# Optimization experiments

Hardware: AMD Instinct MI355X
Metric: run time of the kernel (lower is better)

The kernel has to match this reference:

```python
import jax, jax.numpy as jnp
import numpy as np

B, S, HID = 2, 2048, 4096
H, P, N, G, K = 128, 64, 128, 8, 4      # heads, head_dim, ssm_state, groups, conv kernel
INTER = H * P                           # 8192
CONV_DIM = INTER + 2 * G * N            # 10240
CHUNK = 128
EPS = 1e-5
DT_MIN, DT_MAX = 0.0, 100.0


def setup_inputs() -> dict:
    key = jax.random.key(0)
    ks = jax.random.split(key, 4)
    proj = INTER + CONV_DIM + H
    return {
        "x": jax.random.normal(ks[0], (B, S, HID), jnp.float32),
        "in_proj_w": jax.random.normal(ks[1], (proj, HID), jnp.float32) * 0.02,
        "conv_w": jax.random.normal(ks[2], (CONV_DIM, 1, K), jnp.float32) * 0.2,
        "conv_b": jnp.zeros((CONV_DIM,), jnp.float32),
        "dt_bias": jnp.ones((H,), jnp.float32),
        "A_log": jnp.log(jnp.arange(1, H + 1, dtype=jnp.float32)),
        "D": jnp.ones((H,), jnp.float32),
        "norm_w": jnp.ones((INTER,), jnp.float32),
        "out_proj_w": jax.random.normal(ks[3], (HID, INTER), jnp.float32) * 0.02,
    }


def _segsum(a):
    # a: (..., c) -> (..., c, c); [i, j] = sum_{k=j+1..i} a[k] for i >= j, else -inf
    c = a.shape[-1]
    s = jnp.cumsum(a, axis=-1)
    diff = s[..., :, None] - s[..., None, :]
    mask = jnp.tril(jnp.ones((c, c), dtype=bool))
    return jnp.where(mask, diff, -jnp.inf)


def reference(x, in_proj_w, conv_w, conv_b, dt_bias, A_log, D, norm_w, out_proj_w):
    b, s, _ = x.shape
    proj = jnp.einsum('bsd,ed->bse', x, in_proj_w)
    gate = proj[..., :INTER]
    hBC = proj[..., INTER:INTER + CONV_DIM]
    dt = proj[..., INTER + CONV_DIM:]                       # (b, s, H)

    # depthwise causal conv1d + silu
    xc = jnp.transpose(hBC, (0, 2, 1))                      # (b, conv_dim, s)
    xc = jax.lax.conv_general_dilated(xc, conv_w, (1,), [(K - 1, 0)],
                                      dimension_numbers=('NCH', 'OIH', 'NCH'),
                                      feature_group_count=CONV_DIM)
    xc = xc + conv_b[None, :, None]
    hBC = jax.nn.silu(jnp.transpose(xc, (0, 2, 1)))

    hs = hBC[..., :INTER].reshape(b, s, H, P)
    Bm = hBC[..., INTER:INTER + G * N].reshape(b, s, G, N)
    Cm = hBC[..., INTER + G * N:].reshape(b, s, G, N)

    A = -jnp.exp(A_log)                                     # (H,)
    dt = jnp.clip(jax.nn.softplus(dt + dt_bias), DT_MIN, DT_MAX)

    rep = H // G
    Bh = jnp.repeat(Bm, rep, axis=2)                        # (b, s, H, N)
    Ch = jnp.repeat(Cm, rep, axis=2)

    nc = s // CHUNK
    xch = (hs * dt[..., None]).reshape(b, nc, CHUNK, H, P)  # dt-scaled input, chunked
    Bc = Bh.reshape(b, nc, CHUNK, H, N)
    Cc = Ch.reshape(b, nc, CHUNK, H, N)
    A_dt = (dt * A).reshape(b, nc, CHUNK, H).transpose(0, 3, 1, 2)  # (b, H, nc, c)
    A_cum = jnp.cumsum(A_dt, axis=-1)

    # intra-chunk (diagonal) contribution
    L = jnp.exp(_segsum(A_dt))                              # (b, H, nc, c, c)
    Y_diag = jnp.einsum('bzlhn,bzshn,bhzls,bzshp->bzlhp', Cc, Bc, L, xch)

    # per-chunk final states
    decay_states = jnp.exp(A_cum[..., -1:] - A_cum)         # (b, H, nc, c)
    states = jnp.einsum('bzlhn,bhzl,bzlhp->bzhpn', Bc, decay_states, xch)

    # inter-chunk recurrence (initial state = 0)
    states_p = jnp.concatenate([jnp.zeros_like(states[:, :1]), states], axis=1)  # (b, nc+1, H, P, N)
    A_last = jnp.pad(A_cum[..., -1], ((0, 0), (0, 0), (1, 0)))                   # (b, H, nc+1)
    decay_chunk = jnp.exp(_segsum(A_last))                                        # (b, H, nc+1, nc+1)
    new_states = jnp.einsum('bhzc,bchpn->bzhpn', decay_chunk, states_p)
    prev = new_states[:, :-1]                                # state entering each chunk

    Y_off = jnp.einsum('bzlhn,bzhpn,bhzl->bzlhp', Cc, prev, jnp.exp(A_cum))
    Y = (Y_diag + Y_off).reshape(b, s, H, P) + hs * D[None, None, :, None]
    y = Y.reshape(b, s, INTER)

    # gated grouped RMSNorm (norm_before_gate=False)
    g = y * jax.nn.silu(gate)
    gg = g.reshape(b, s, G, INTER // G)
    var = jnp.mean(gg * gg, axis=-1, keepdims=True)
    gg = gg * jax.lax.rsqrt(var + EPS)
    out = gg.reshape(b, s, INTER) * norm_w

    return jnp.einsum('bsi,oi->bso', out, out_proj_w)
```

## Files before the change

kernel.cpp:

```cpp
#include <hip/hip_runtime.h>
#include <hip/hip_bf16.h>
#include <cstdint>
#include <cstddef>

#define DEVI __device__ __forceinline__

#define BB 2
#define S_LEN 2048
#define HID_DIM 4096
#define NH 128
#define PD 64
#define NS 128
#define NG 8
#define INTER 8192
#define CONVD 10240
#define PROJ 18560
#define PROJP 18688
#define NC 16
#define BS 4096
#define GN 1024

using short8 = __attribute__((ext_vector_type(8))) short;
using short4v = __attribute__((ext_vector_type(4))) short;
using f32x4  = __attribute__((ext_vector_type(4))) float;
using bf16x8 = __attribute__((ext_vector_type(8))) __bf16;

DEVI float bf2f(short u) {
  union { unsigned int i; float f; } v;
  v.i = ((unsigned int)(unsigned short)u) << 16;
  return v.f;
}
DEVI short f2bf(float f) {
  union { float ff; unsigned int i; } v; v.ff = f;
  unsigned int x = v.i;
  return (short)((x + 0x7fffu + ((x >> 16) & 1u)) >> 16);
}
DEVI f32x4 mfma16(short8 a, short8 b, f32x4 c) {
  return __builtin_amdgcn_mfma_f32_16x16x32_bf16(
      __builtin_bit_cast(bf16x8, a), __builtin_bit_cast(bf16x8, b), c, 0, 0, 0);
}
DEVI void gl_lds16(const short* g, short* l) {
  __builtin_amdgcn_global_load_lds(
      (const __attribute__((address_space(1))) void*)g,
      (__attribute__((address_space(3))) void*)l, 16, 0, 0);
}
DEVI float sigmoidf_(float x) { return 1.f / (1.f + __expf(-x)); }

__global__ __launch_bounds__(256) void cvt_f32_bf16_k(const float* __restrict__ in,
                                                      short* __restrict__ out, size_t n) {
  size_t i = ((size_t)blockIdx.x * 256 + threadIdx.x) * 8;
  if (i + 8 > n) return;
  float4 a = *(const float4*)(in + i);
  float4 b = *(const float4*)(in + i + 4);
  short8 o;
  o[0] = f2bf(a.x); o[1] = f2bf(a.y); o[2] = f2bf(a.z); o[3] = f2bf(a.w);
  o[4] = f2bf(b.x); o[5] = f2bf(b.y); o[6] = f2bf(b.z); o[7] = f2bf(b.w);
  *(short8*)(out + i) = o;
}


#define STG(ISB, BUF, KH, TILE) do { \
  const short* _src = (ISB) ? Bt : A; \
  const int _r0 = (ISB) ? n0 : m0; \
  short* _lb = lds_ + ((ISB) ? 32768 : 0) + ((BUF)*2+(KH))*8192; \
  const int _kt = (TILE)*64 + (KH)*32; \
  { int _row = (wid*2)*16 + srow; int _sl = sps ^ ((_row>>1)&3); \
    gl_lds16(_src + (size_t)(_r0+_row)*K + _kt + _sl*8, _lb + (wid*2)*512); } \
  { int _row = (wid*2+1)*16 + srow; int _sl = sps ^ ((_row>>1)&3); \
    gl_lds16(_src + (size_t)(_r0+_row)*K + _kt + _sl*8, _lb + (wid*2+1)*512); } \
} while(0)

#define VM4 asm volatile("s_waitcnt vmcnt(4)" ::: "memory")
#define VM0 asm volatile("s_waitcnt vmcnt(0)" ::: "memory")

#define LDAF(DST, BUF, KH, MIH) do { \
  _Pragma("unroll") \
  for (int _m = 0; _m < 4; ++_m) { \
    int _row = wr*128 + ((MIH)*4+_m)*16 + fr; \
    DST[_m] = *(const short8*)(lds_ + ((BUF)*2+(KH))*8192 + _row*32 + ((slot ^ ((_row>>1)&3))<<3)); \
  } \
} while(0)

#define LDBF(DST, BUF, KH) do { \
  _Pragma("unroll") \
  for (int _n = 0; _n < 4; ++_n) { \
    int _row = wc*64 + _n*16 + fr; \
    DST[_n] = *(const short8*)(lds_ + 32768 + ((BUF)*2+(KH))*8192 + _row*32 + ((slot ^ ((_row>>1)&3))<<3)); \
  } \
} while(0)

#define MFMA16X(MIH, AF, BF) do { \
  _Pragma("unroll") \
  for (int _m = 0; _m < 4; ++_m) \
    _Pragma("unroll") \
    for (int _n = 0; _n < 4; ++_n) \
      acc[(MIH)*4+_m][_n] = mfma16(AF[_m], BF[_n], acc[(MIH)*4+_m][_n]); \
} while(0)

#define ITER(CB, NB, TNEXT, DOSTG, VMW) do { \
  if (DOSTG) { STG(0, NB, 0, TNEXT); STG(1, NB, 0, TNEXT); } \
  VMW; \
  __builtin_amdgcn_s_barrier(); \
  LDAF(af0, CB, 0, 0); LDAF(af1, CB, 1, 0); \
  LDBF(bf0, CB, 0); LDBF(bf1, CB, 1); \
  __builtin_amdgcn_s_setprio(1); \
  MFMA16X(0, af0, bf0); \
  MFMA16X(0, af1, bf1); \
  __builtin_amdgcn_s_setprio(0); \
  if (DOSTG) { STG(0, NB, 1, TNEXT); STG(1, NB, 1, TNEXT); } \
  LDAF(af0, CB, 0, 1); LDAF(af1, CB, 1, 1); \
  __builtin_amdgcn_s_setprio(1); \
  MFMA16X(1, af0, bf0); \
  MFMA16X(1, af1, bf1); \
  __builtin_amdgcn_s_setprio(0); \
  asm volatile("s_waitcnt lgkmcnt(0)" ::: "memory"); \
  __builtin_amdgcn_s_barrier(); \
} while(0)

template<int CB16>
__global__ __launch_bounds__(512, 2) void gemm256_k(const short* __restrict__ A,
                                                    const short* __restrict__ Bt,
                                                    void* __restrict__ Cout,
                                                    int Nstride, int K, int ntn) {
  __shared__ short lds_[65536];
  const int tid = threadIdx.x, wid = tid >> 6, lane = tid & 63;
  const int nwg = gridDim.x, orig = blockIdx.x;
  const int swz = (orig & 7) * (nwg >> 3) + (orig >> 3);
  const int per_group = ntn << 3;
  const int group = swz / per_group;
  const int rem = swz - group * per_group;
  const int m0 = (group * 8 + (rem & 7)) * 256;
  const int n0 = (rem >> 3) * 256;
  const int wr = wid >> 2, wc = wid & 3;
  const int fr = lane & 15, slot = lane >> 4;
  const int srow = lane >> 2, sps = lane & 3;

  f32x4 acc[8][4] = {};
  short8 af0[4], af1[4], bf0[4], bf1[4];
  const int NT = K >> 6;

  STG(0, 0, 0, 0); STG(1, 0, 0, 0); STG(0, 0, 1, 0); STG(1, 0, 1, 0);

  for (int ii = 0; ii < (NT >> 1) - 1; ++ii) {
    const int t = 2 * ii;
    ITER(0, 1, t + 1, 1, VM4);
    ITER(1, 0, t + 2, 1, VM4);
  }
  ITER(0, 1, NT - 1, 1, VM4);
  ITER(1, 0, 0, 0, VM0);

  const int er = (lane >> 4) * 4, ec = lane & 15;
  if (CB16) {
    short* C = (short*)Cout;
#pragma unroll
    for (int mi = 0; mi < 8; ++mi)
#pragma unroll
      for (int j = 0; j < 4; ++j) {
        size_t base = (size_t)(m0 + wr * 128 + mi * 16 + er + j) * Nstride + n0 + wc * 64 + ec;
#pragma unroll
        for (int ni = 0; ni < 4; ++ni) C[base + ni * 16] = f2bf(acc[mi][ni][j]);
      }
  } else {
    float* C = (float*)Cout;
#pragma unroll
    for (int mi = 0; mi < 8; ++mi)
#pragma unroll
      for (int j = 0; j < 4; ++j) {
        size_t base = (size_t)(m0 + wr * 128 + mi * 16 + er + j) * Nstride + n0 + wc * 64 + ec;
#pragma unroll
        for (int ni = 0; ni < 4; ++ni) C[base + ni * 16] = acc[mi][ni][j];
      }
  }
}

__global__ __launch_bounds__(256) void conv_silu_k(const short* __restrict__ projb,
                                                   const float* __restrict__ convw,
                                                   const float* __restrict__ convb,
                                                   short* __restrict__ hbc) {
  const int c = blockIdx.x * 256 + threadIdx.x;
  const int s0 = blockIdx.y * 256;
  const int b = blockIdx.z;
  const size_t rb = (size_t)b * S_LEN;
  const float* wp = convw + (size_t)c * 4;
  const float w0 = wp[0], w1 = wp[1], w2 = wp[2], w3 = wp[3];
  const float bias = convb[c];
  const short* pcol = projb + INTER + c;
  float x1 = 0.f, x2 = 0.f, x3 = 0.f;
  if (s0 > 0) {
    x3 = bf2f(pcol[(rb + s0 - 3) * PROJP]);
    x2 = bf2f(pcol[(rb + s0 - 2) * PROJP]);
    x1 = bf2f(pcol[(rb + s0 - 1) * PROJP]);
  }
  for (int s = s0; s < s0 + 256; ++s) {
    float v = bf2f(pcol[(rb + s) * PROJP]);
    float acc = bias + w0 * x3 + w1 * x2 + w2 * x1 + w3 * v;
    float o = acc * sigmoidf_(acc);
    hbc[(rb + s) * CONVD + c] = f2bf(o);
    x3 = x2; x2 = x1; x1 = v;
  }
}

__global__ __launch_bounds__(128) void acum_k(const short* __restrict__ projb,
                                              const float* __restrict__ dt_bias,
                                              const float* __restrict__ A_log,
                                              float* __restrict__ dtT,
                                              float* __restrict__ acum) {
  const int l = threadIdx.x;
  const int z = blockIdx.x, h = blockIdx.y, b = blockIdx.z;
  const float A = -__expf(A_log[h]);
  __shared__ float sv[128];
  const int r = b * S_LEN + z * 128 + l;
  float xv = bf2f(projb[(size_t)r * PROJP + INTER + CONVD + h]) + dt_bias[h];
  float sp = (xv > 20.f) ? xv : log1pf(__expf(xv));
  sp = fminf(fmaxf(sp, 0.f), 100.f);
  const size_t base = ((size_t)(b * NH + h)) * S_LEN + z * 128;
  dtT[base + l] = sp;
  sv[l] = sp * A;
  __syncthreads();
  for (int off = 1; off < 128; off <<= 1) {
    float t = (l >= off) ? sv[l - off] : 0.f;
    __syncthreads();
    sv[l] += t;
    __syncthreads();
  }
  acum[base + l] = sv[l];
}

__global__ __launch_bounds__(512) void states_k(const short* __restrict__ hbc,
                                                const float* __restrict__ dtT,
                                                const float* __restrict__ acum,
                                                float* __restrict__ states) {
  __shared__ short sBT[128 * 136];
  __shared__ short sxdt2[2][64 * 136];
  const int tid = threadIdx.x, wid = tid >> 6, lane = tid & 63;
  const int g = blockIdx.x, z = blockIdx.y, b = blockIdx.z;
  const size_t srow0 = (size_t)(b * S_LEN + z * 128);
  const short* hrow = hbc + srow0 * CONVD;

  {
    const int l = tid & 127, n0b = (tid >> 7) * 32;
    const short* src = hrow + (size_t)l * CONVD + INTER + g * NS + n0b;
    short8 v0 = *(const short8*)(src);
    short8 v1 = *(const short8*)(src + 8);
    short8 v2 = *(const short8*)(src + 16);
    short8 v3 = *(const short8*)(src + 24);
#pragma unroll
    for (int j = 0; j < 8; ++j) {
      sBT[(n0b + j) * 136 + l] = v0[j];
      sBT[(n0b + 8 + j) * 136 + l] = v1[j];
      sBT[(n0b + 16 + j) * 136 + l] = v2[j];
      sBT[(n0b + 24 + j) * 136 + l] = v3[j];
    }
  }

  const int fr = lane & 15, fk8 = (lane >> 4) * 8;
  const int er = (lane >> 4) * 4, ec = lane & 15;
  const int pband = (wid & 3) * 16, nhalf = (wid >> 2) * 64;
  const int s2 = tid & 63, p0w = (tid >> 6) * 8;

  float cdv0, cdv1; short8 cr0, cr1;
  {
    const int h = g * 16;
    const float* acg = acum + ((size_t)(b * NH + h)) * S_LEN + z * 128;
    const float* dts = dtT + ((size_t)(b * NH + h)) * S_LEN + z * 128;
    const float acL = acg[127];
    cdv0 = dts[2 * s2] * __expf(acL - acg[2 * s2]);
    cdv1 = dts[2 * s2 + 1] * __expf(acL - acg[2 * s2 + 1]);
    const short* rsrc = hrow + (size_t)(2 * s2) * CONVD + (size_t)h * PD + p0w;
    cr0 = *(const short8*)(rsrc);
    cr1 = *(const short8*)(rsrc + CONVD);
  }
  {
    unsigned int* x32 = (unsigned int*)sxdt2[0];
#pragma unroll
    for (int j = 0; j < 8; ++j) {
      unsigned int lo = (unsigned short)f2bf(bf2f(cr0[j]) * cdv0);
      unsigned int hi = (unsigned short)f2bf(bf2f(cr1[j]) * cdv1);
      x32[(p0w + j) * 68 + s2] = lo | (hi << 16);
    }
  }
  __syncthreads();

  for (int hh = 0; hh < 16; ++hh) {
    const int h = g * 16 + hh;
    float ndv0 = 0.f, ndv1 = 0.f; short8 nr0, nr1;
    if (hh < 15) {
      const int h2 = h + 1;
      const float* acg = acum + ((size_t)(b * NH + h2)) * S_LEN + z * 128;
      const float* dts = dtT + ((size_t)(b * NH + h2)) * S_LEN + z * 128;
      const float acL = acg[127];
      ndv0 = dts[2 * s2] * __expf(acL - acg[2 * s2]);
      ndv1 = dts[2 * s2 + 1] * __expf(acL - acg[2 * s2 + 1]);
      const short* rsrc = hrow + (size_t)(2 * s2) * CONVD + (size_t)h2 * PD + p0w;
      nr0 = *(const short8*)(rsrc);
      nr1 = *(const short8*)(rsrc + CONVD);
    }
    const short* sx = sxdt2[hh & 1];
    f32x4 st[4] = {};
#pragma unroll
    for (int kk = 0; kk < 4; ++kk) {
      short8 a = *(const short8*)(sx + (pband + fr) * 136 + kk * 32 + fk8);
#pragma unroll
      for (int ni = 0; ni < 4; ++ni) {
        short8 bb = *(const short8*)(sBT + (nhalf + ni * 16 + fr) * 136 + kk * 32 + fk8);
        st[ni] = mfma16(a, bb, st[ni]);
      }
    }
    float* stp = states + (((size_t)(b * NC + z)) * NH + h) * (size_t)(NS * PD);
#pragma unroll
    for (int ni = 0; ni < 4; ++ni)
#pragma unroll
      for (int j = 0; j < 4; ++j)
        stp[(pband + er + j) * NS + nhalf + ni * 16 + ec] = st[ni][j];
    if (hh < 15) {
      unsigned int* x32 = (unsigned int*)sxdt2[(hh + 1) & 1];
#pragma unroll
      for (int j = 0; j < 8; ++j) {
        unsigned int lo = (unsigned short)f2bf(bf2f(nr0[j]) * ndv0);
        unsigned int hi = (unsigned short)f2bf(bf2f(nr1[j]) * ndv1);
        x32[(p0w + j) * 68 + s2] = lo | (hi << 16);
      }
    }
    __syncthreads();
  }
}

__global__ __launch_bounds__(256) void scan_k(float* __restrict__ states,
                                              const float* __restrict__ acum) {
  const int h = blockIdx.x, b = blockIdx.y;
  const int tid = threadIdx.x;
  float* stp = states + ((size_t)(b * NC * NH) + h) * (size_t)(NS * PD);
  const size_t cst = (size_t)NH * NS * PD;
  const float* ac = acum + ((size_t)(b * NH + h)) * S_LEN;
  float E[32];
#pragma unroll
  for (int i = 0; i < 32; ++i) E[i] = 0.f;
  const int n = tid & 127, pg = tid >> 7;
  for (int zz = 0; zz < NC; ++zz) {
    float* sz = stp + (size_t)zz * cst;
    short* pvb = (short*)sz;
    float tmp[32];
#pragma unroll
    for (int i = 0; i < 32; ++i) tmp[i] = sz[i * 256 + tid];
    __syncthreads();
    float dec = __expf(ac[zz * 128 + 127]);
#pragma unroll
    for (int i = 0; i < 32; ++i) {
      int p = i * 2 + pg;
      pvb[p * 128 + n] = f2bf(E[i]);
      E[i] = dec * E[i] + tmp[i];
    }
    __syncthreads();
  }
}

#define RDSW(BUF, ROWBASE, KK) \
  (*(const short8*)((BUF) + ((ROWBASE) + fr) * 128 + ((((KK) * 4 + slot4) ^ sw7) << 3)))

#define WRX(DST, D0, D1, R0, R1) do { \
  unsigned int* _x = (unsigned int*)(DST); \
  _Pragma("unroll") \
  for (int _j = 0; _j < 8; ++_j) { \
    unsigned int _lo = (unsigned short)f2bf(bf2f(R0[_j]) * (D0)); \
    unsigned int _hi = (unsigned short)f2bf(bf2f(R1[_j]) * (D1)); \
    _x[(p0w + _j) * 64 + ((((s2 >> 2) ^ _j) << 2) | (s2 & 3))] = _lo | (_hi << 16); \
  } \
} while (0)

#define WRP(DST, P0, P1) do { \
  int _p = tid >> 3; int _s0 = (tid & 7) * 2; int _m = _p & 7; \
  *(short8*)((DST) + _p * 128 + ((_s0 ^ _m) << 3)) = P0; \
  *(short8*)((DST) + _p * 128 + (((_s0 + 1) ^ _m) << 3)) = P1; \
} while (0)

#define LOADH_Y(H, DT0, DT1, ACS, ACL, R0, R1, P0, P1) do { \
  const float* _ac = acum + ((size_t)(b * NH + (H))) * S_LEN + z * 128; \
  const float* _dts = dtT + ((size_t)(b * NH + (H))) * S_LEN + z * 128; \
  DT0 = _dts[2 * s2]; DT1 = _dts[2 * s2 + 1]; \
  _Pragma("unroll") \
  for (int _si = 0; _si < 8; ++_si) ACS[_si] = _ac[_si * 16 + ec]; \
  _Pragma("unroll") \
  for (int _j = 0; _j < 4; ++_j) ACL[_j] = _ac[lrow + er + _j]; \
  const short* _rs = hrow + (size_t)(2 * s2) * CONVD + (size_t)(H) * PD + p0w; \
  R0 = *(const short8*)(_rs); R1 = *(const short8*)(_rs + CONVD); \
  const short* _pv = (const short*)(states + (((size_t)(b * NC + z)) * NH + (H)) * (size_t)(NS * PD)); \
  P0 = *(const short8*)(_pv + tid * 16); P1 = *(const short8*)(_pv + tid * 16 + 8); \
} while (0)

__global__ __launch_bounds__(512) void yfull_k(const short* __restrict__ hbc,
                                               const short* __restrict__ projb,
                                               const float* __restrict__ dtT,
                                               const float* __restrict__ acum,
                                               const float* __restrict__ states,
                                               const float* __restrict__ Dv,
                                               const float* __restrict__ norm_w,
                                               short* __restrict__ normed) {
  __shared__ short lds[66560];
  __shared__ float sScale[128];
  __shared__ float sNW[1024];
  short* sC = lds;
  short* sB = lds + 16384;
  short* sx0 = lds + 32768;
  short* sp0 = lds + 40960;
  const int tid = threadIdx.x, wid = tid >> 6, lane = tid & 63;
  short* sPw = lds + 49152 + wid * 2176;
  const int g = blockIdx.x, z = blockIdx.y, b = blockIdx.z;
  const size_t srow0 = (size_t)(b * S_LEN + z * 128);
  const short* hrow = hbc + srow0 * CONVD;

  {
    const int slot_g = (lane & 15) ^ (((wid & 1) << 2) | (lane >> 4));
    const int n0_ = slot_g * 8;
#pragma unroll
    for (int it = 0; it < 4; ++it) {
      int s = it * 32 + wid * 4 + (lane >> 4);
      gl_lds16(hrow + (size_t)s * CONVD + INTER + GN + g * NS + n0_, sC + (it * 32 + wid * 4) * 128);
      gl_lds16(hrow + (size_t)s * CONVD + INTER + g * NS + n0_, sB + (it * 32 + wid * 4) * 128);
    }
  }
  for (int i = tid; i < 1024; i += 512) sNW[i] = norm_w[g * 1024 + i];
  __syncthreads();

  const int fr = lane & 15, fk8 = (lane >> 4) * 8;
  const int slot4 = lane >> 4, sw7 = lane & 7;
  const int er = (lane >> 4) * 4, ec = lane & 15;
  const int lrow = wid * 16;
  const int s2 = tid & 63, p0w = (tid >> 6) * 8;

  float cdt0, cdt1, cacS[8], cacl[4];
  short8 cr0, cr1, cp0, cp1;
  LOADH_Y(g * 16, cdt0, cdt1, cacS, cacl, cr0, cr1, cp0, cp1);

  f32x4 sc[8] = {};
#pragma unroll
  for (int kk = 0; kk < 4; ++kk) {
    short8 a = RDSW(sC, lrow, kk);
#pragma unroll
    for (int si = 0; si < 8; ++si) {
      short8 bv = RDSW(sB, si * 16, kk);
      sc[si] = mfma16(a, bv, sc[si]);
    }
  }
  WRX(sx0, cdt0, cdt1, cr0, cr1);
  WRP(sp0, cp0, cp1);
  __syncthreads();

  float rssq[4] = {0.f, 0.f, 0.f, 0.f};

  for (int hh = 0; hh < 16; ++hh) {
    const int h = g * 16 + hh;
    float ndt0 = 0.f, ndt1 = 0.f, nacS[8], nacl[4];
    short8 nr0, nr1, np0, np1;
    if (hh < 15) LOADH_Y(h + 1, ndt0, ndt1, nacS, nacl, nr0, nr1, np0, np1);

    short* sx = (hh & 1) ? sB : sx0;
    short* sp = (hh & 1) ? (sB + 8192) : sp0;

#pragma unroll
    for (int j = 0; j < 4; ++j) {
      int lloc = er + j;
      float acl = cacl[j];
#pragma unroll
      for (int si = 0; si < 8; ++si) {
        int sI = si * 16 + ec;
        float v = (sI <= lrow + lloc) ? sc[si][j] * __expf(acl - cacS[si]) : 0.f;
        sPw[lloc * 136 + sI] = f2bf(v);
      }
    }
    f32x4 yd[4] = {}, yo[4] = {};
#pragma unroll
    for (int kk = 0; kk < 4; ++kk) {
      short8 ap = *(const short8*)(sPw + fr * 136 + kk * 32 + fk8);
      short8 acf = RDSW(sC, lrow, kk);
#pragma unroll
      for (int ni = 0; ni < 4; ++ni) {
        short8 bv = RDSW(sx, ni * 16, kk);
        yd[ni] = mfma16(ap, bv, yd[ni]);
        short8 bp = RDSW(sp, ni * 16, kk);
        yo[ni] = mfma16(acf, bp, yo[ni]);
      }
    }
    const float Dh = Dv[h];
#pragma unroll
    for (int j = 0; j < 4; ++j) {
      int l = lrow + er + j;
      float e_ac = __expf(cacl[j]);
#pragma unroll
      for (int ni = 0; ni < 4; ++ni) {
        int p = ni * 16 + ec;
        float hs = bf2f(hrow[(size_t)l * CONVD + (size_t)h * PD + p]);
        float y = yd[ni][j] + yo[ni][j] * e_ac + hs * Dh;
        float gate = bf2f(projb[(srow0 + l) * (size_t)PROJP + (size_t)h * PD + p]);
        float gg = y * gate * sigmoidf_(gate);
        normed[(srow0 + l) * (size_t)INTER + (size_t)h * PD + p] = f2bf(gg);
        rssq[j] += gg * gg;
      }
    }
    if (hh < 15) {
      short* nx = (hh & 1) ? sx0 : sB;
      short* npv = (hh & 1) ? sp0 : (sB + 8192);
      WRX(nx, ndt0, ndt1, nr0, nr1);
      WRP(npv, np0, np1);
      cdt0 = ndt0; cdt1 = ndt1; cr0 = nr0; cr1 = nr1; cp0 = np0; cp1 = np1;
#pragma unroll
      for (int si = 0; si < 8; ++si) cacS[si] = nacS[si];
#pragma unroll
      for (int j = 0; j < 4; ++j) cacl[j] = nacl[j];
    }
    __syncthreads();
  }

#pragma unroll
  for (int j = 0; j < 4; ++j) {
#pragma unroll
    for (int m = 1; m <= 8; m <<= 1) rssq[j] += __shfl_xor(rssq[j], m, 64);
  }
  if (ec == 0) {
#pragma unroll
    for (int j = 0; j < 4; ++j) sScale[lrow + er + j] = rsqrtf(rssq[j] * (1.f / 1024.f) + 1e-5f);
  }
  __syncthreads();

  for (int e = tid * 8; e < 128 * 1024; e += 4096) {
    int row = e >> 10, ch = e & 1023;
    short* gp = normed + (srow0 + row) * (size_t)INTER + g * 1024 + ch;
    short8 gv = *(const short8*)(gp);
    float scl = sScale[row];
    short8 o;
#pragma unroll
    for (int q = 0; q < 8; ++q) o[q] = f2bf(bf2f(gv[q]) * scl * sNW[ch + q]);
    *(short8*)(gp) = o;
  }
}

extern "C" void kernel_launch(void* const* d_in, const int* in_sizes, int n_in,
                              void* d_out, int out_size, void* d_ws, size_t ws_size,
                              hipStream_t stream) {
  const float* x     = (const float*)d_in[0];
  const float* w1    = (const float*)d_in[1];
  const float* convw = (const float*)d_in[2];
  const float* convb = (const float*)d_in[3];
  const float* dtb   = (const float*)d_in[4];
  const float* alog  = (const float*)d_in[5];
  const float* Dv    = (const float*)d_in[6];
  const float* nw    = (const float*)d_in[7];
  const float* w2    = (const float*)d_in[8];
  float* out = (float*)d_out;

  char* ws = (char*)d_ws;
  size_t off = 0;
  float* dtT = (float*)(ws + off);  off += (size_t)BB * NH * S_LEN * 4;
  float* acum = (float*)(ws + off); off += (size_t)BB * NH * S_LEN * 4;
  short* xb = (short*)(ws + off);   off += (size_t)BS * HID_DIM * 2;
  char* w1region = ws + off;        off += (size_t)PROJP * HID_DIM * 2;
  short* w1b = (short*)w1region;
  short* normed = (short*)w1region;
  short* w2b = (short*)(w1region + (size_t)BS * INTER * 2);
  short* projb = (short*)(ws + off); off += (size_t)BS * PROJP * 2;
  short* hbc = (short*)(ws + off);   off += (size_t)BS * CONVD * 2;
  float* states = (float*)(ws + off); off += (size_t)BB * NC * NH * NS * PD * 4;

  const size_t nx = (size_t)BS * HID_DIM;
  const size_t nw1 = (size_t)PROJ * HID_DIM;
  const size_t nw2 = (size_t)HID_DIM * INTER;

  cvt_f32_bf16_k<<<dim3(nx / 2048), 256, 0, stream>>>(x, xb, nx);
  cvt_f32_bf16_k<<<dim3(nw1 / 2048), 256, 0, stream>>>(w1, w1b, nw1);

  gemm256_k<1><<<dim3(16 * 73), 512, 0, stream>>>(xb, w1b, projb, PROJP, HID_DIM, 73);

  cvt_f32_bf16_k<<<dim3(nw2 / 2048), 256, 0, stream>>>(w2, w2b, nw2);

  conv_silu_k<<<dim3(CONVD / 256, S_LEN / 256, BB), 256, 0, stream>>>(projb, convw, convb, hbc);
  acum_k<<<dim3(NC, NH, BB), 128, 0, stream>>>(projb, dtb, alog, dtT, acum);

  states_k<<<dim3(NG, NC, BB), 512, 0, stream>>>(hbc, dtT, acum, states);
  scan_k<<<dim3(NH, BB), 256, 0, stream>>>(states, acum);
  yfull_k<<<dim3(NG, NC, BB), 512, 0, stream>>>(hbc, projb, dtT, acum, states, Dv, nw, normed);

  gemm256_k<0><<<dim3(16 * 16), 512, 0, stream>>>(normed, w2b, out, HID_DIM, INTER, 16);
}
```

Before: 1.172 ms.

## Load GEMM B operand directly from global into registers, bypassing LDS

The B tile in the 256x256 bf16 GEMM is no longer staged through shared memory. Each wave now reads its B fragments straight from global memory into double-buffered registers, one tile ahead. Only A still goes through LDS, so shared memory use is halved and the B LDS reads and swizzle are gone. In exchange, register pressure rises, waves holding the same columns load the same B data twice, the per-lane global reads are narrow and strided by row, and the vmcnt wait threshold is retuned to cover the extra loads in flight.

After: 1.663 ms. +41.9%, slower.

```diff
diff --git a/kernel.cpp b/kernel.cpp
--- a/kernel.cpp
+++ b/kernel.cpp
@@ -59,18 +59,16 @@
 }
 
 
-#define STG(ISB, BUF, KH, TILE) do { \
-  const short* _src = (ISB) ? Bt : A; \
-  const int _r0 = (ISB) ? n0 : m0; \
-  short* _lb = lds_ + ((ISB) ? 32768 : 0) + ((BUF)*2+(KH))*8192; \
+#define STGA(BUF, KH, TILE) do { \
+  short* _lb = lds_ + ((BUF)*2+(KH))*8192; \
   const int _kt = (TILE)*64 + (KH)*32; \
   { int _row = (wid*2)*16 + srow; int _sl = sps ^ ((_row>>1)&3); \
-    gl_lds16(_src + (size_t)(_r0+_row)*K + _kt + _sl*8, _lb + (wid*2)*512); } \
+    gl_lds16(A + (size_t)(m0+_row)*K + _kt + _sl*8, _lb + (wid*2)*512); } \
   { int _row = (wid*2+1)*16 + srow; int _sl = sps ^ ((_row>>1)&3); \
-    gl_lds16(_src + (size_t)(_r0+_row)*K + _kt + _sl*8, _lb + (wid*2+1)*512); } \
+    gl_lds16(A + (size_t)(m0+_row)*K + _kt + _sl*8, _lb + (wid*2+1)*512); } \
 } while(0)
 
-#define VM4 asm volatile("s_waitcnt vmcnt(4)" ::: "memory")
+#define VM12 asm volatile("s_waitcnt vmcnt(12)" ::: "memory")
 #define VM0 asm volatile("s_waitcnt vmcnt(0)" ::: "memory")
 
 #define LDAF(DST, BUF, KH, MIH) do { \
@@ -81,38 +79,38 @@
   } \
 } while(0)
 
-#define LDBF(DST, BUF, KH) do { \
+#define LDBG(DST, T) do { \
   _Pragma("unroll") \
   for (int _n = 0; _n < 4; ++_n) { \
-    int _row = wc*64 + _n*16 + fr; \
-    DST[_n] = *(const short8*)(lds_ + 32768 + ((BUF)*2+(KH))*8192 + _row*32 + ((slot ^ ((_row>>1)&3))<<3)); \
+    const short* _p = Bt + (size_t)(n0 + wc*64 + _n*16 + fr) * K + (T)*64 + fk8g; \
+    DST[_n] = *(const short8*)(_p); \
+    DST[_n + 4] = *(const short8*)(_p + 32); \
   } \
 } while(0)
 
-#define MFMA16X(MIH, AF, BF) do { \
+#define MFMA16XP(MIH, AF, BP) do { \
   _Pragma("unroll") \
   for (int _m = 0; _m < 4; ++_m) \
     _Pragma("unroll") \
     for (int _n = 0; _n < 4; ++_n) \
-      acc[(MIH)*4+_m][_n] = mfma16(AF[_m], BF[_n], acc[(MIH)*4+_m][_n]); \
+      acc[(MIH)*4+_m][_n] = mfma16(AF[_m], (BP)[_n], acc[(MIH)*4+_m][_n]); \
 } while(0)
 
-#define ITER(CB, NB, TNEXT, DOSTG, VMW) do { \
-  if (DOSTG) { STG(0, NB, 0, TNEXT); STG(1, NB, 0, TNEXT); } \
+#define ITERG(CB, NB, TN, BARR, DOSTG, DOLDB, VMW) do { \
+  if (DOSTG) { STGA(NB, 0, TN); STGA(NB, 1, TN); } \
   VMW; \
   __builtin_amdgcn_s_barrier(); \
   LDAF(af0, CB, 0, 0); LDAF(af1, CB, 1, 0); \
-  LDBF(bf0, CB, 0); LDBF(bf1, CB, 1); \
   __builtin_amdgcn_s_setprio(1); \
-  MFMA16X(0, af0, bf0); \
-  MFMA16X(0, af1, bf1); \
+  MFMA16XP(0, af0, BARR); \
+  MFMA16XP(0, af1, (BARR) + 4); \
   __builtin_amdgcn_s_setprio(0); \
-  if (DOSTG) { STG(0, NB, 1, TNEXT); STG(1, NB, 1, TNEXT); } \
   LDAF(af0, CB, 0, 1); LDAF(af1, CB, 1, 1); \
   __builtin_amdgcn_s_setprio(1); \
-  MFMA16X(1, af0, bf0); \
-  MFMA16X(1, af1, bf1); \
+  MFMA16XP(1, af0, BARR); \
+  MFMA16XP(1, af1, (BARR) + 4); \
   __builtin_amdgcn_s_setprio(0); \
+  if (DOLDB) LDBG(BARR, (TN) + 1); \
   asm volatile("s_waitcnt lgkmcnt(0)" ::: "memory"); \
   __builtin_amdgcn_s_barrier(); \
 } while(0)
@@ -122,7 +120,7 @@
                                                     const short* __restrict__ Bt,
                                                     void* __restrict__ Cout,
                                                     int Nstride, int K, int ntn) {
-  __shared__ short lds_[65536];
+  __shared__ short lds_[32768];
   const int tid = threadIdx.x, wid = tid >> 6, lane = tid & 63;
   const int nwg = gridDim.x, orig = blockIdx.x;
   const int swz = (orig & 7) * (nwg >> 3) + (orig >> 3);
@@ -133,21 +131,25 @@
   const int n0 = (rem >> 3) * 256;
   const int wr = wid >> 2, wc = wid & 3;
   const int fr = lane & 15, slot = lane >> 4;
+  const int fk8g = slot * 8;
   const int srow = lane >> 2, sps = lane & 3;
 
   f32x4 acc[8][4] = {};
-  short8 af0[4], af1[4], bf0[4], bf1[4];
+  short8 af0[4], af1[4];
+  short8 bB0[8], bB1[8];
   const int NT = K >> 6;
 
-  STG(0, 0, 0, 0); STG(1, 0, 0, 0); STG(0, 0, 1, 0); STG(1, 0, 1, 0);
-
-  for (int ii = 0; ii < (NT >> 1) - 1; ++ii) {
+  LDBG(bB0, 0);
+  STGA(0, 0, 0); STGA(0, 1, 0);
+  LDBG(bB1, 1);
+
+  for (int ii = 0; ii < (NT - 2) >> 1; ++ii) {
     const int t = 2 * ii;
-    ITER(0, 1, t + 1, 1, VM4);
-    ITER(1, 0, t + 2, 1, VM4);
-  }
-  ITER(0, 1, NT - 1, 1, VM4);
-  ITER(1, 0, 0, 0, VM0);
+    ITERG(0, 1, t + 1, bB0, 1, 1, VM12);
+    ITERG(1, 0, t + 2, bB1, 1, 1, VM12);
+  }
+  ITERG(0, 1, NT - 1, bB0, 1, 0, VM12);
+  ITERG(1, 0, 0, bB1, 0, 0, VM0);
 
   const int er = (lane >> 4) * 4, ec = lane & 15;
   if (CB16) {
```
